# Kernel tuning notes

Measured on AMD Instinct MI355X. Metric: run time of the kernel, lower is better.

Reference implementation:

```python
import jax, jax.numpy as jnp
import numpy as np

VOCAB, HIDDEN, BATCH, TLEN = 32000, 512, 32, 64


def _lstm_cell(x, h, c, Wih, Whh, bih, bhh):
    # PyTorch LSTMCell gate order: i, f, g, o
    g = x @ Wih.T + bih + h @ Whh.T + bhh  # [B, 4H]
    i, f, gg, o = jnp.split(g, 4, axis=-1)
    i = jax.nn.sigmoid(i)
    f = jax.nn.sigmoid(f)
    gg = jnp.tanh(gg)
    o = jax.nn.sigmoid(o)
    c2 = f * c + i * gg
    h2 = o * jnp.tanh(c2)
    return h2, c2


def setup_inputs() -> dict:
    key = jax.random.key(0)
    ks = jax.random.split(key, 16)
    s = 0.02
    inp = {
        "inputs": jax.random.randint(ks[0], (1, BATCH), 0, VOCAB),
        "hiddens": jax.random.normal(ks[1], (BATCH, HIDDEN), jnp.float32),
        "target_sequences": jax.random.randint(ks[2], (BATCH, TLEN), 0, VOCAB),
        "use_tf": 1,
        "emb": jax.random.normal(ks[3], (VOCAB, HIDDEN), jnp.float32) * s,
        "W_ih1": jax.random.normal(ks[4], (4 * HIDDEN, HIDDEN), jnp.float32) * s,
        "W_hh1": jax.random.normal(ks[5], (4 * HIDDEN, HIDDEN), jnp.float32) * s,
        "b_ih1": jax.random.normal(ks[6], (4 * HIDDEN,), jnp.float32) * s,
        "b_hh1": jax.random.normal(ks[7], (4 * HIDDEN,), jnp.float32) * s,
        "W_ih2": jax.random.normal(ks[8], (4 * HIDDEN, HIDDEN), jnp.float32) * s,
        "W_hh2": jax.random.normal(ks[9], (4 * HIDDEN, HIDDEN), jnp.float32) * s,
        "b_ih2": jax.random.normal(ks[10], (4 * HIDDEN,), jnp.float32) * s,
        "b_hh2": jax.random.normal(ks[11], (4 * HIDDEN,), jnp.float32) * s,
        "W_out": jax.random.normal(ks[12], (VOCAB, HIDDEN), jnp.float32) * s,
        "b_out": jax.random.normal(ks[13], (VOCAB,), jnp.float32) * s,
    }
    return inp


def reference(inputs, hiddens, target_sequences, use_tf, emb, W_ih1, W_hh1,
              b_ih1, b_hh1, W_ih2, W_hh2, b_ih2, b_hh2, W_out, b_out):
    # Teacher-forcing path (use_tf is a static Python int; dropout p=0 -> identity).
    B = inputs.shape[1]
    H = hiddens.shape[1]
    # step i consumes: emb(inputs) for i=0, emb(target[:, i-1]) for i>0
    e0 = emb[inputs[0]]                              # [B, H]
    et = emb[target_sequences.T[:-1]]                # [T-1, B, H]
    x_seq = jnp.concatenate([e0[None], et], axis=0)  # [T, B, H]

    c1 = jnp.zeros((B, H), hiddens.dtype)
    h2 = jnp.zeros((B, H), hiddens.dtype)
    c2 = jnp.zeros((B, H), hiddens.dtype)

    def step(carry, x):
        h1, c1, h2, c2 = carry
        h1, c1 = _lstm_cell(x, h1, c1, W_ih1, W_hh1, b_ih1, b_hh1)
        h2, c2 = _lstm_cell(h1, h2, c2, W_ih2, W_hh2, b_ih2, b_hh2)
        probs = jax.nn.softmax(h2 @ W_out.T + b_out, axis=-1)  # [B, V]
        return (h1, c1, h2, c2), probs

    (h1, c1, h2, c2), output = jax.lax.scan(step, (hiddens, c1, h2, c2), x_seq)
    return output, h1  # output: [T, B, V]
```

## Files before the change

kernel.cpp:

```cpp
#include <hip/hip_runtime.h>
#include <stdint.h>


constexpr int kH = 512;
constexpr int kB = 32;
constexpr int kT = 64;
constexpr int kV = 32000;
constexpr int kG = 2048;
constexpr int kNWG = 256;
constexpr int kWS = 129;

typedef __attribute__((ext_vector_type(4))) float f4;
typedef __attribute__((ext_vector_type(8))) short short8;
typedef unsigned long long u64;

struct us4 { unsigned short x, y, z, w; };

__device__ inline unsigned short f2bf(float x) {
  union { float f; unsigned u; } c; c.f = x;
  unsigned r = c.u + 0x7fffu + ((c.u >> 16) & 1u);
  return (unsigned short)(r >> 16);
}
__device__ inline float sigm(float x) { return 1.0f / (1.0f + expf(-x)); }

__global__ void k_init(float* __restrict__ buf2, float* __restrict__ rowsum,
                       int* __restrict__ flags ) {
  int id = blockIdx.x * 256 + threadIdx.x;
  f4 z = {0.f, 0.f, 0.f, 0.f};
  if (id < 8192) ((f4*)buf2)[id] = z;
  if (id < 2048) rowsum[id] = 0.f;
  if (id < 512)  flags[id] = 0;
}

__global__ void k_wcvt(const float* __restrict__ W, unsigned short* __restrict__ Wu) {
  const int total = kV * kH / 4;
  for (int i = blockIdx.x * blockDim.x + threadIdx.x; i < total;
       i += gridDim.x * blockDim.x) {
    f4 v = ((const f4*)W)[i];
    us4 o = {f2bf(v.x), f2bf(v.y), f2bf(v.z), f2bf(v.w)};
    ((us4*)Wu)[i] = o;
  }
}

__global__ __launch_bounds__(256) void k_xg1(
    const int* __restrict__ inputs, const int* __restrict__ tseq,
    const float* __restrict__ emb, const float* __restrict__ Wih1,
    const float* __restrict__ bih1, const float* __restrict__ bhh1,
    float* __restrict__ Xg1T) {
  __shared__ float Xs[kB * kH];
  int tid = threadIdx.x;
  int t = blockIdx.x, jb = blockIdx.y;
  for (int i = tid; i < kB * kH / 4; i += 256) {
    int b = i >> 7;
    int tok = (t == 0) ? inputs[b] : tseq[b * kT + (t - 1)];
    ((f4*)Xs)[i] = ((const f4*)(emb + (size_t)tok * kH))[i & 127];
  }
  __syncthreads();
  int j2 = tid & 31, bq = tid >> 5;
  int j0 = jb * 64 + j2 * 2;
  int b0 = bq * 4;
  const f4* w0 = (const f4*)(Wih1 + (size_t)j0 * kH);
  const f4* w1 = (const f4*)(Wih1 + (size_t)(j0 + 1) * kH);
  float acc0[4] = {0.f, 0.f, 0.f, 0.f};
  float acc1[4] = {0.f, 0.f, 0.f, 0.f};
  #pragma unroll 2
  for (int k4 = 0; k4 < 128; ++k4) {
    f4 a0 = w0[k4], a1 = w1[k4];
    #pragma unroll
    for (int bb = 0; bb < 4; ++bb) {
      f4 x = ((const f4*)Xs)[(b0 + bb) * 128 + k4];
      acc0[bb] += a0.x * x.x + a0.y * x.y + a0.z * x.z + a0.w * x.w;
      acc1[bb] += a1.x * x.x + a1.y * x.y + a1.z * x.z + a1.w * x.w;
    }
  }
  float bj0 = bih1[j0] + bhh1[j0];
  float bj1 = bih1[j0 + 1] + bhh1[j0 + 1];
  f4 s0 = {acc0[0] + bj0, acc0[1] + bj0, acc0[2] + bj0, acc0[3] + bj0};
  f4 s1 = {acc1[0] + bj1, acc1[1] + bj1, acc1[2] + bj1, acc1[3] + bj1};
  float* o = Xg1T + ((size_t)t * kG + j0) * kB + b0;
  *(f4*)o = s0;
  *(f4*)(o + kB) = s1;
}

__device__ inline void postc(int* cnt) {
  __syncthreads();
  if (threadIdx.x == 0)
    __hip_atomic_fetch_add(&cnt[(blockIdx.x & 7) << 5], 1, __ATOMIC_RELAXED,
                           __HIP_MEMORY_SCOPE_AGENT);
}
__device__ inline void waitc(int* cnt, int target) {
  if (threadIdx.x < 64) {
    int lane = threadIdx.x;
    for (;;) {
      int v = (lane < 8)
                  ? __hip_atomic_load(&cnt[lane << 5], __ATOMIC_RELAXED,
                                      __HIP_MEMORY_SCOPE_AGENT)
                  : 0;
      v += __shfl_xor(v, 1);
      v += __shfl_xor(v, 2);
      v += __shfl_xor(v, 4);
      if (__shfl(v, 0) >= target) break;
      __builtin_amdgcn_s_sleep(2);
    }
  }
  __syncthreads();
}

__device__ inline void stage_coh(float* __restrict__ smem, const float* src) {
  const u64* s8 = (const u64*)src;
  #pragma unroll
  for (int i = 0; i < 16; ++i) {
    int idx = threadIdx.x + (i << 8);
    u64 lo = __hip_atomic_load((u64*)&s8[idx * 2], __ATOMIC_RELAXED,
                               __HIP_MEMORY_SCOPE_AGENT);
    u64 hi = __hip_atomic_load((u64*)&s8[idx * 2 + 1], __ATOMIC_RELAXED,
                               __HIP_MEMORY_SCOPE_AGENT);
    int b_ = idx >> 7, k4 = idx & 127;
    union { u64 u[2]; f4 v; } cv; cv.u[0] = lo; cv.u[1] = hi;
    ((f4*)smem)[(b_ << 7) + (k4 ^ (b_ & 7))] = cv.v;
  }
}
__device__ inline void stage_plain(float* __restrict__ smem,
                                   const float* __restrict__ src) {
  const f4* s4 = (const f4*)src;
  #pragma unroll
  for (int i = 0; i < 16; ++i) {
    int idx = threadIdx.x + (i << 8);
    int b_ = idx >> 7, k4 = idx & 127;
    ((f4*)smem)[(b_ << 7) + (k4 ^ (b_ & 7))] = s4[idx];
  }
}

__device__ inline float redk(float s) {
  s += __shfl_xor(s, 1);
  s += __shfl_xor(s, 2);
  s += __shfl_xor(s, 4);
  return s;
}

__global__ __launch_bounds__(256, 1) void k_serial(
    const float* __restrict__ hiddens, const float* __restrict__ Xg1T,
    const float* __restrict__ Whh1, const float* __restrict__ Wih2,
    const float* __restrict__ Whh2, const float* __restrict__ bih2,
    const float* __restrict__ bhh2,
    float* __restrict__ buf1, float* __restrict__ buf2,
    unsigned short* __restrict__ H2u, float* __restrict__ outTail,
    int* __restrict__ cntA, int* __restrict__ cntB) {
  __shared__ float smemh[kB * kH];
  __shared__ float wlds[24 * 4 * kWS];
  const int tid = threadIdx.x, w = blockIdx.x;
  const int lane = tid & 63, wv = tid >> 6;
  const int ks = lane & 7;
  const int nl = (lane >> 3) & 1;
  const int bq = lane >> 4;
  const int bp = (wv << 2) | bq;
  const int b0 = bp << 1, b1 = b0 + 1;
  const int b0off = b0 << 7, b1off = b1 << 7;
  const int b0sw = b0 & 7, b1sw = b1 & 7;
  const int n = (w << 1) + nl;

  {
    f4* wl = (f4*)wlds;
    #pragma unroll
    for (int i = 0; i < 12; ++i) {
      int idx = tid + (i << 8);
      int row = idx >> 7, k4 = idx & 127;
      int m = row >> 3, jjr = row & 7;
      int jr = ((jjr >> 1) << 9) + (w << 1) + (jjr & 1);
      const float* src = (m == 0) ? Whh1 : (m == 1) ? Whh2 : Wih2;
      wl[row * kWS + k4] = ((const f4*)(src + (size_t)jr * kH))[k4];
    }
  }
  const f4* wr_hh1[4];
  const f4* wr_hh2[4];
  const f4* wr_ih2[4];
  #pragma unroll
  for (int gg = 0; gg < 4; ++gg) {
    int row = 2 * gg + nl;
    wr_hh1[gg] = (const f4*)wlds + (0 * 8 + row) * kWS;
    wr_hh2[gg] = (const f4*)wlds + (1 * 8 + row) * kWS;
    wr_ih2[gg] = (const f4*)wlds + (2 * 8 + row) * kWS;
  }
  float bj[4];
  #pragma unroll
  for (int gg = 0; gg < 4; ++gg)
    bj[gg] = bih2[(gg << 9) + n] + bhh2[(gg << 9) + n];

  const f4* hsm = (const f4*)smemh;
  float c1a = 0.f, c1b = 0.f, c2a = 0.f, c2b = 0.f;
  const f4 z4 = {0.f, 0.f, 0.f, 0.f};

  stage_plain(smemh, hiddens);
  __syncthreads();
  for (int t = 0; t < kT; ++t) {
    float* h1w = buf1 + (t & 1) * 16384;
    float* h2w = buf2 + (t & 1) * 16384;
    const float* h2r = buf2 + ((t + 1) & 1) * 16384;

    union { u64 u; float f[2]; } xv[4];
    const float* xbase = Xg1T + ((size_t)t * kG + n) * kB + b0;
    #pragma unroll
    for (int gg = 0; gg < 4; ++gg)
      xv[gg].u = *(const u64*)(xbase + (size_t)(gg << 9) * kB);

    f4 a00 = z4, a01 = z4, a10 = z4, a11 = z4, a20 = z4, a21 = z4,
       a30 = z4, a31 = z4;
    #pragma unroll 4
    for (int kk = 0; kk < 16; ++kk) {
      int k4 = (kk << 3) | ks;
      f4 h0v = hsm[b0off + (k4 ^ b0sw)];
      f4 h1v = hsm[b1off + (k4 ^ b1sw)];
      f4 w0 = wr_hh1[0][k4], w1 = wr_hh1[1][k4];
      f4 w2 = wr_hh1[2][k4], w3 = wr_hh1[3][k4];
      a00 += w0 * h0v; a01 += w0 * h1v;
      a10 += w1 * h0v; a11 += w1 * h1v;
      a20 += w2 * h0v; a21 += w2 * h1v;
      a30 += w3 * h0v; a31 += w3 * h1v;
    }
    float G00 = redk(a00.x + a00.y + a00.z + a00.w) + xv[0].f[0];
    float G01 = redk(a01.x + a01.y + a01.z + a01.w) + xv[0].f[1];
    float G10 = redk(a10.x + a10.y + a10.z + a10.w) + xv[1].f[0];
    float G11 = redk(a11.x + a11.y + a11.z + a11.w) + xv[1].f[1];
    float G20 = redk(a20.x + a20.y + a20.z + a20.w) + xv[2].f[0];
    float G21 = redk(a21.x + a21.y + a21.z + a21.w) + xv[2].f[1];
    float G30 = redk(a30.x + a30.y + a30.z + a30.w) + xv[3].f[0];
    float G31 = redk(a31.x + a31.y + a31.z + a31.w) + xv[3].f[1];
    c1a = sigm(G10) * c1a + sigm(G00) * tanhf(G20);
    float hn0 = sigm(G30) * tanhf(c1a);
    c1b = sigm(G11) * c1b + sigm(G01) * tanhf(G21);
    float hn1 = sigm(G31) * tanhf(c1b);
    float hp0 = __shfl(hn0, lane ^ 8);
    float hp1 = __shfl(hn1, lane ^ 8);
    if ((lane & 15) == 0) {
      union { float f[2]; u64 u; } p0, p1;
      p0.f[0] = hn0; p0.f[1] = hp0;
      p1.f[0] = hn1; p1.f[1] = hp1;
      __hip_atomic_store((u64*)(h1w + b0 * kH + 2 * w), p0.u, __ATOMIC_RELAXED,
                         __HIP_MEMORY_SCOPE_AGENT);
      __hip_atomic_store((u64*)(h1w + b1 * kH + 2 * w), p1.u, __ATOMIC_RELAXED,
                         __HIP_MEMORY_SCOPE_AGENT);
      if (t == kT - 1) {
        *(u64*)(outTail + b0 * kH + 2 * w) = p0.u;
        *(u64*)(outTail + b1 * kH + 2 * w) = p1.u;
      }
    }
    postc(cntA);
    waitc(cntB, 256 * t);

    stage_coh(smemh, h2r);
    __syncthreads();
    a00 = z4; a01 = z4; a10 = z4; a11 = z4;
    a20 = z4; a21 = z4; a30 = z4; a31 = z4;
    #pragma unroll 4
    for (int kk = 0; kk < 16; ++kk) {
      int k4 = (kk << 3) | ks;
      f4 h0v = hsm[b0off + (k4 ^ b0sw)];
      f4 h1v = hsm[b1off + (k4 ^ b1sw)];
      f4 w0 = wr_hh2[0][k4], w1 = wr_hh2[1][k4];
      f4 w2 = wr_hh2[2][k4], w3 = wr_hh2[3][k4];
      a00 += w0 * h0v; a01 += w0 * h1v;
      a10 += w1 * h0v; a11 += w1 * h1v;
      a20 += w2 * h0v; a21 += w2 * h1v;
      a30 += w3 * h0v; a31 += w3 * h1v;
    }
    waitc(cntA, 256 * (t + 1));

    stage_coh(smemh, h1w);
    __syncthreads();
    #pragma unroll 4
    for (int kk = 0; kk < 16; ++kk) {
      int k4 = (kk << 3) | ks;
      f4 h0v = hsm[b0off + (k4 ^ b0sw)];
      f4 h1v = hsm[b1off + (k4 ^ b1sw)];
      f4 w0 = wr_ih2[0][k4], w1 = wr_ih2[1][k4];
      f4 w2 = wr_ih2[2][k4], w3 = wr_ih2[3][k4];
      a00 += w0 * h0v; a01 += w0 * h1v;
      a10 += w1 * h0v; a11 += w1 * h1v;
      a20 += w2 * h0v; a21 += w2 * h1v;
      a30 += w3 * h0v; a31 += w3 * h1v;
    }
    G00 = redk(a00.x + a00.y + a00.z + a00.w) + bj[0];
    G01 = redk(a01.x + a01.y + a01.z + a01.w) + bj[0];
    G10 = redk(a10.x + a10.y + a10.z + a10.w) + bj[1];
    G11 = redk(a11.x + a11.y + a11.z + a11.w) + bj[1];
    G20 = redk(a20.x + a20.y + a20.z + a20.w) + bj[2];
    G21 = redk(a21.x + a21.y + a21.z + a21.w) + bj[2];
    G30 = redk(a30.x + a30.y + a30.z + a30.w) + bj[3];
    G31 = redk(a31.x + a31.y + a31.z + a31.w) + bj[3];
    c2a = sigm(G10) * c2a + sigm(G00) * tanhf(G20);
    float h2n0 = sigm(G30) * tanhf(c2a);
    c2b = sigm(G11) * c2b + sigm(G01) * tanhf(G21);
    float h2n1 = sigm(G31) * tanhf(c2b);
    float h2p0 = __shfl(h2n0, lane ^ 8);
    float h2p1 = __shfl(h2n1, lane ^ 8);
    if ((lane & 15) == 0) {
      union { float f[2]; u64 u; } p0, p1;
      p0.f[0] = h2n0; p0.f[1] = h2p0;
      p1.f[0] = h2n1; p1.f[1] = h2p1;
      __hip_atomic_store((u64*)(h2w + b0 * kH + 2 * w), p0.u, __ATOMIC_RELAXED,
                         __HIP_MEMORY_SCOPE_AGENT);
      __hip_atomic_store((u64*)(h2w + b1 * kH + 2 * w), p1.u, __ATOMIC_RELAXED,
                         __HIP_MEMORY_SCOPE_AGENT);
      unsigned bf0 = ((unsigned)f2bf(h2p0) << 16) | f2bf(h2n0);
      unsigned bf1 = ((unsigned)f2bf(h2p1) << 16) | f2bf(h2n1);
      *(unsigned*)(H2u + ((size_t)t * kB + b0) * kH + 2 * w) = bf0;
      *(unsigned*)(H2u + ((size_t)t * kB + b1) * kH + 2 * w) = bf1;
    }
    postc(cntB);
  }
}

__global__ __launch_bounds__(256) void k_vocab(
    const unsigned short* __restrict__ H2u, const unsigned short* __restrict__ Wu,
    const float* __restrict__ bout, float* __restrict__ out,
    float* __restrict__ rowsum) {
  const int lane = threadIdx.x & 63, wv = threadIdx.x >> 6;
  const int wm = wv >> 1, wn = wv & 1;
  const int r16 = lane & 15, quad = lane >> 4;
  const int mBase = blockIdx.y * 128 + wm * 64;
  const int nBase = blockIdx.x * 128 + wn * 64;
  f4 acc[4][4];
  #pragma unroll
  for (int a = 0; a < 4; ++a)
    #pragma unroll
    for (int c = 0; c < 4; ++c) acc[a][c] = (f4){0.f, 0.f, 0.f, 0.f};
  for (int kb = 0; kb < 16; ++kb) {
    int k0 = kb * 32 + quad * 8;
    short8 af[4], bf[4];
    #pragma unroll
    for (int mt = 0; mt < 4; ++mt)
      af[mt] = *(const short8*)(H2u + (size_t)(mBase + mt * 16 + r16) * kH + k0);
    #pragma unroll
    for (int nt = 0; nt < 4; ++nt)
      bf[nt] = *(const short8*)(Wu + (size_t)(nBase + nt * 16 + r16) * kH + k0);
    #pragma unroll
    for (int mt = 0; mt < 4; ++mt)
      #pragma unroll
      for (int nt = 0; nt < 4; ++nt)
        acc[mt][nt] = __builtin_amdgcn_mfma_f32_16x16x32_bf16(
            af[mt], bf[nt], acc[mt][nt], 0, 0, 0);
  }
  float bo[4];
  #pragma unroll
  for (int nt = 0; nt < 4; ++nt) bo[nt] = bout[nBase + nt * 16 + r16];
  #pragma unroll
  for (int mt = 0; mt < 4; ++mt) {
    #pragma unroll
    for (int r = 0; r < 4; ++r) {
      int row = mBase + mt * 16 + quad * 4 + r;
      float s = 0.f;
      #pragma unroll
      for (int nt = 0; nt < 4; ++nt) {
        float p = __expf(acc[mt][nt][r] + bo[nt]);
        out[(size_t)row * kV + nBase + nt * 16 + r16] = p;
        s += p;
      }
      s += __shfl_xor(s, 1);
      s += __shfl_xor(s, 2);
      s += __shfl_xor(s, 4);
      s += __shfl_xor(s, 8);
      if (r16 == 0) atomicAdd(&rowsum[row], s);
    }
  }
}

__global__ void k_scale(float* __restrict__ out, const float* __restrict__ rowsum) {
  const unsigned total4 = (unsigned)(kT * kB) * (kV / 4);
  unsigned stride = gridDim.x * blockDim.x;
  for (unsigned i = blockIdx.x * blockDim.x + threadIdx.x; i < total4; i += stride) {
    unsigned row = i / (kV / 4);
    float inv = 1.0f / rowsum[row];
    f4 v = ((const f4*)out)[i];
    ((f4*)out)[i] = v * inv;
  }
}

extern "C" void kernel_launch(void* const* d_in, const int* in_sizes, int n_in,
                              void* d_out, int out_size, void* d_ws, size_t ws_size,
                              hipStream_t stream) {
  (void)in_sizes; (void)n_in; (void)out_size; (void)ws_size;
  const int*   inputs  = (const int*)d_in[0];
  const float* hiddens = (const float*)d_in[1];
  const int*   tseq    = (const int*)d_in[2];
  const float* emb  = (const float*)d_in[4];
  const float* Wih1 = (const float*)d_in[5];
  const float* Whh1 = (const float*)d_in[6];
  const float* bih1 = (const float*)d_in[7];
  const float* bhh1 = (const float*)d_in[8];
  const float* Wih2 = (const float*)d_in[9];
  const float* Whh2 = (const float*)d_in[10];
  const float* bih2 = (const float*)d_in[11];
  const float* bhh2 = (const float*)d_in[12];
  const float* Wout = (const float*)d_in[13];
  const float* bout = (const float*)d_in[14];

  float* ws = (float*)d_ws;
  float* Xg1T = ws;
  float* buf1 = ws + 4194304;
  float* buf2 = ws + 4227072;
  unsigned short* H2u = (unsigned short*)(ws + 4259840);
  unsigned short* Wu  = (unsigned short*)(ws + 4784128);
  float* rowsum = ws + 12976128;
  int* flags = (int*)(ws + 12978176);
  int* cntA = flags;
  int* cntB = flags + 256;

  float* out = (float*)d_out;
  float* outTail = out + (size_t)kT * kB * kV;

  hipLaunchKernelGGL(k_init, dim3(32), dim3(256), 0, stream, buf2, rowsum, flags);
  hipLaunchKernelGGL(k_wcvt, dim3(1024), dim3(256), 0, stream, Wout, Wu);
  hipLaunchKernelGGL(k_xg1, dim3(64, 32), dim3(256), 0, stream,
                     inputs, tseq, emb, Wih1, bih1, bhh1, Xg1T);
  hipLaunchKernelGGL(k_serial, dim3(kNWG), dim3(256), 0, stream,
                     hiddens, Xg1T, Whh1, Wih2, Whh2, bih2, bhh2,
                     buf1, buf2, H2u, outTail, cntA, cntB);
  hipLaunchKernelGGL(k_vocab, dim3(kV / 128, 16), dim3(256), 0, stream,
                     H2u, Wu, bout, out, rowsum);
  hipLaunchKernelGGL(k_scale, dim3(2048), dim3(256), 0, stream, out, rowsum);
}
```

Before: 2.072 ms.

## Fuse vocab projection and softmax normalization into the persistent recurrent kernel

Removes the separate vocab GEMM and scale kernels. Each of 250 persistent workgroups now computes a 32x128 logits tile for step t-1 while waiting on the recurrence, and writes normalized probabilities for step t-2 after the existing inter-WG barrier. Partial row sums go to per-WG slots and are summed on read. This hides vocab work behind the latency-bound serial loop and avoids writing then re-reading the unnormalized output. In exchange it adds MFMA work and register pressure inside the critical serial loop, which may lengthen each step.

```diff
diff --git a/kernel.cpp b/kernel.cpp
--- a/kernel.cpp
+++ b/kernel.cpp
@@ -9,6 +9,7 @@
 constexpr int kG = 2048;
 constexpr int kNWG = 256;
 constexpr int kWS = 129;
+constexpr int kNV = 250;
 
 typedef __attribute__((ext_vector_type(4))) float f4;
 typedef __attribute__((ext_vector_type(8))) short short8;
@@ -23,12 +24,12 @@
 }
 __device__ inline float sigm(float x) { return 1.0f / (1.0f + expf(-x)); }
 
-__global__ void k_init(float* __restrict__ buf2, float* __restrict__ rowsum,
+__global__ void k_init(float* __restrict__ buf2, float* __restrict__ rs,
                        int* __restrict__ flags ) {
   int id = blockIdx.x * 256 + threadIdx.x;
   f4 z = {0.f, 0.f, 0.f, 0.f};
   if (id < 8192) ((f4*)buf2)[id] = z;
-  if (id < 2048) rowsum[id] = 0.f;
+  ((f4*)rs)[id] = z;
   if (id < 512)  flags[id] = 0;
 }
 
@@ -144,10 +145,14 @@
     const float* __restrict__ Whh2, const float* __restrict__ bih2,
     const float* __restrict__ bhh2,
     float* __restrict__ buf1, float* __restrict__ buf2,
-    unsigned short* __restrict__ H2u, float* __restrict__ outTail,
+    unsigned short* __restrict__ H2u,
+    const unsigned short* __restrict__ Wu, const float* __restrict__ bout,
+    float* __restrict__ outP, float* __restrict__ rs,
+    float* __restrict__ outTail,
     int* __restrict__ cntA, int* __restrict__ cntB) {
   __shared__ float smemh[kB * kH];
   __shared__ float wlds[24 * 4 * kWS];
+  __shared__ float sinv[4][32];
   const int tid = threadIdx.x, w = blockIdx.x;
   const int lane = tid & 63, wv = tid >> 6;
   const int ks = lane & 7;
@@ -158,6 +163,10 @@
   const int b0off = b0 << 7, b1off = b1 << 7;
   const int b0sw = b0 & 7, b1sw = b1 & 7;
   const int n = (w << 1) + nl;
+  const int r16 = lane & 15, quad = lane >> 4;
+  const int colb = w * 128 + wv * 32;
+  float bo0 = 0.f, bo1 = 0.f;
+  if (w < kNV) { bo0 = bout[colb + r16]; bo1 = bout[colb + 16 + r16]; }
 
   {
     f4* wl = (f4*)wlds;
@@ -189,6 +198,83 @@
   const f4* hsm = (const f4*)smemh;
   float c1a = 0.f, c1b = 0.f, c2a = 0.f, c2b = 0.f;
   const f4 z4 = {0.f, 0.f, 0.f, 0.f};
+  f4 p00 = z4, p01 = z4, p10 = z4, p11 = z4;
+
+  auto vocab_tile = [&](int tt) {
+    p00 = z4; p01 = z4; p10 = z4; p11 = z4;
+    const unsigned short* A0 = H2u + ((size_t)tt * kB + r16) * kH;
+    const unsigned short* A1 = A0 + (size_t)16 * kH;
+    const unsigned short* B0 = Wu + (size_t)(colb + r16) * kH;
+    const unsigned short* B1 = B0 + (size_t)16 * kH;
+    #pragma unroll 2
+    for (int kb = 0; kb < 16; ++kb) {
+      int k0 = kb * 32 + quad * 8;
+      union { u64 u[2]; short8 s; } a0, a1;
+      a0.u[0] = __hip_atomic_load((const u64*)(A0 + k0), __ATOMIC_RELAXED,
+                                  __HIP_MEMORY_SCOPE_AGENT);
+      a0.u[1] = __hip_atomic_load((const u64*)(A0 + k0 + 4), __ATOMIC_RELAXED,
+                                  __HIP_MEMORY_SCOPE_AGENT);
+      a1.u[0] = __hip_atomic_load((const u64*)(A1 + k0), __ATOMIC_RELAXED,
+                                  __HIP_MEMORY_SCOPE_AGENT);
+      a1.u[1] = __hip_atomic_load((const u64*)(A1 + k0 + 4), __ATOMIC_RELAXED,
+                                  __HIP_MEMORY_SCOPE_AGENT);
+      short8 vb0 = *(const short8*)(B0 + k0);
+      short8 vb1 = *(const short8*)(B1 + k0);
+      p00 = __builtin_amdgcn_mfma_f32_16x16x32_bf16(a0.s, vb0, p00, 0, 0, 0);
+      p01 = __builtin_amdgcn_mfma_f32_16x16x32_bf16(a0.s, vb1, p01, 0, 0, 0);
+      p10 = __builtin_amdgcn_mfma_f32_16x16x32_bf16(a1.s, vb0, p10, 0, 0, 0);
+      p11 = __builtin_amdgcn_mfma_f32_16x16x32_bf16(a1.s, vb1, p11, 0, 0, 0);
+    }
+    float* rsb = rs + tt * 1024 + (w & 31) * 32;
+    #pragma unroll
+    for (int r = 0; r < 4; ++r) {
+      float e0 = __expf(p00[r] + bo0), e1 = __expf(p01[r] + bo1);
+      p00[r] = e0; p01[r] = e1;
+      float s = e0 + e1;
+      s += __shfl_xor(s, 1); s += __shfl_xor(s, 2);
+      s += __shfl_xor(s, 4); s += __shfl_xor(s, 8);
+      if (r16 == 0) atomicAdd(&rsb[quad * 4 + r], s);
+      float f0 = __expf(p10[r] + bo0), f1 = __expf(p11[r] + bo1);
+      p10[r] = f0; p11[r] = f1;
+      float u = f0 + f1;
+      u += __shfl_xor(u, 1); u += __shfl_xor(u, 2);
+      u += __shfl_xor(u, 4); u += __shfl_xor(u, 8);
+      if (r16 == 0) atomicAdd(&rsb[16 + quad * 4 + r], u);
+    }
+  };
+  auto scale_store = [&](int ts) {
+    const float* rb = rs + ts * 1024;
+    if (lane < 32) {
+      float s = 0.f;
+      #pragma unroll 8
+      for (int sl = 0; sl < 32; ++sl) {
+        union { unsigned u; float f; } cv;
+        cv.u = __hip_atomic_load((const unsigned*)(rb + sl * 32 + lane),
+                                 __ATOMIC_RELAXED, __HIP_MEMORY_SCOPE_AGENT);
+        s += cv.f;
+      }
+      sinv[wv][lane] = 1.0f / s;
+    }
+    __syncthreads();
+    float* ob = outP + (size_t)ts * kB * kV + colb;
+    #pragma unroll
+    for (int r = 0; r < 4; ++r) {
+      {
+        int rr = quad * 4 + r;
+        float inv = sinv[wv][rr];
+        float* orow = ob + (size_t)rr * kV;
+        orow[r16] = p00[r] * inv;
+        orow[16 + r16] = p01[r] * inv;
+      }
+      {
+        int rr = 16 + quad * 4 + r;
+        float inv = sinv[wv][rr];
+        float* orow = ob + (size_t)rr * kV;
+        orow[r16] = p10[r] * inv;
+        orow[16 + r16] = p11[r] * inv;
+      }
+    }
+  };
 
   stage_plain(smemh, hiddens);
   __syncthreads();
@@ -232,23 +318,28 @@
     float hp0 = __shfl(hn0, lane ^ 8);
     float hp1 = __shfl(hn1, lane ^ 8);
     if ((lane & 15) == 0) {
-      union { float f[2]; u64 u; } p0, p1;
-      p0.f[0] = hn0; p0.f[1] = hp0;
-      p1.f[0] = hn1; p1.f[1] = hp1;
-      __hip_atomic_store((u64*)(h1w + b0 * kH + 2 * w), p0.u, __ATOMIC_RELAXED,
+      union { float f[2]; u64 u; } q0, q1;
+      q0.f[0] = hn0; q0.f[1] = hp0;
+      q1.f[0] = hn1; q1.f[1] = hp1;
+      __hip_atomic_store((u64*)(h1w + b0 * kH + 2 * w), q0.u, __ATOMIC_RELAXED,
                          __HIP_MEMORY_SCOPE_AGENT);
-      __hip_atomic_store((u64*)(h1w + b1 * kH + 2 * w), p1.u, __ATOMIC_RELAXED,
+      __hip_atomic_store((u64*)(h1w + b1 * kH + 2 * w), q1.u, __ATOMIC_RELAXED,
                          __HIP_MEMORY_SCOPE_AGENT);
       if (t == kT - 1) {
-        *(u64*)(outTail + b0 * kH + 2 * w) = p0.u;
-        *(u64*)(outTail + b1 * kH + 2 * w) = p1.u;
+        *(u64*)(outTail + b0 * kH + 2 * w) = q0.u;
+        *(u64*)(outTail + b1 * kH + 2 * w) = q1.u;
       }
     }
     postc(cntA);
     waitc(cntB, 256 * t);
 
+    if (t >= 2 && w < kNV) scale_store(t - 2);
+
     stage_coh(smemh, h2r);
     __syncthreads();
+
+    if (t >= 1 && w < kNV) vocab_tile(t - 1);
+
     a00 = z4; a01 = z4; a10 = z4; a11 = z4;
     a20 = z4; a21 = z4; a30 = z4; a31 = z4;
     #pragma unroll 4
@@ -294,85 +385,29 @@
     float h2p0 = __shfl(h2n0, lane ^ 8);
     float h2p1 = __shfl(h2n1, lane ^ 8);
     if ((lane & 15) == 0) {
-      union { float f[2]; u64 u; } p0, p1;
-      p0.f[0] = h2n0; p0.f[1] = h2p0;
-      p1.f[0] = h2n1; p1.f[1] = h2p1;
-      __hip_atomic_store((u64*)(h2w + b0 * kH + 2 * w), p0.u, __ATOMIC_RELAXED,
+      union { float f[2]; u64 u; } q0, q1;
+      q0.f[0] = h2n0; q0.f[1] = h2p0;
+      q1.f[0] = h2n1; q1.f[1] = h2p1;
+      __hip_atomic_store((u64*)(h2w + b0 * kH + 2 * w), q0.u, __ATOMIC_RELAXED,
                          __HIP_MEMORY_SCOPE_AGENT);
-      __hip_atomic_store((u64*)(h2w + b1 * kH + 2 * w), p1.u, __ATOMIC_RELAXED,
+      __hip_atomic_store((u64*)(h2w + b1 * kH + 2 * w), q1.u, __ATOMIC_RELAXED,
                          __HIP_MEMORY_SCOPE_AGENT);
       unsigned bf0 = ((unsigned)f2bf(h2p0) << 16) | f2bf(h2n0);
       unsigned bf1 = ((unsigned)f2bf(h2p1) << 16) | f2bf(h2n1);
-      *(unsigned*)(H2u + ((size_t)t * kB + b0) * kH + 2 * w) = bf0;
-      *(unsigned*)(H2u + ((size_t)t * kB + b1) * kH + 2 * w) = bf1;
+      __hip_atomic_store((unsigned*)(H2u + ((size_t)t * kB + b0) * kH + 2 * w),
+                         bf0, __ATOMIC_RELAXED, __HIP_MEMORY_SCOPE_AGENT);
+      __hip_atomic_store((unsigned*)(H2u + ((size_t)t * kB + b1) * kH + 2 * w),
+                         bf1, __ATOMIC_RELAXED, __HIP_MEMORY_SCOPE_AGENT);
     }
     postc(cntB);
   }
-}
-
-__global__ __launch_bounds__(256) void k_vocab(
-    const unsigned short* __restrict__ H2u, const unsigned short* __restrict__ Wu,
-    const float* __restrict__ bout, float* __restrict__ out,
-    float* __restrict__ rowsum) {
-  const int lane = threadIdx.x & 63, wv = threadIdx.x >> 6;
-  const int wm = wv >> 1, wn = wv & 1;
-  const int r16 = lane & 15, quad = lane >> 4;
-  const int mBase = blockIdx.y * 128 + wm * 64;
-  const int nBase = blockIdx.x * 128 + wn * 64;
-  f4 acc[4][4];
-  #pragma unroll
-  for (int a = 0; a < 4; ++a)
-    #pragma unroll
-    for (int c = 0; c < 4; ++c) acc[a][c] = (f4){0.f, 0.f, 0.f, 0.f};
-  for (int kb = 0; kb < 16; ++kb) {
-    int k0 = kb * 32 + quad * 8;
-    short8 af[4], bf[4];
-    #pragma unroll
-    for (int mt = 0; mt < 4; ++mt)
-      af[mt] = *(const short8*)(H2u + (size_t)(mBase + mt * 16 + r16) * kH + k0);
-    #pragma unroll
-    for (int nt = 0; nt < 4; ++nt)
-      bf[nt] = *(const short8*)(Wu + (size_t)(nBase + nt * 16 + r16) * kH + k0);
-    #pragma unroll
-    for (int mt = 0; mt < 4; ++mt)
-      #pragma unroll
-      for (int nt = 0; nt < 4; ++nt)
-        acc[mt][nt] = __builtin_amdgcn_mfma_f32_16x16x32_bf16(
-            af[mt], bf[nt], acc[mt][nt], 0, 0, 0);
-  }
-  float bo[4];
-  #pragma unroll
-  for (int nt = 0; nt < 4; ++nt) bo[nt] = bout[nBase + nt * 16 + r16];
-  #pragma unroll
-  for (int mt = 0; mt < 4; ++mt) {
-    #pragma unroll
-    for (int r = 0; r < 4; ++r) {
-      int row = mBase + mt * 16 + quad * 4 + r;
-      float s = 0.f;
-      #pragma unroll
-      for (int nt = 0; nt < 4; ++nt) {
-        float p = __expf(acc[mt][nt][r] + bo[nt]);
-        out[(size_t)row * kV + nBase + nt * 16 + r16] = p;
-        s += p;
-      }
-      s += __shfl_xor(s, 1);
-      s += __shfl_xor(s, 2);
-      s += __shfl_xor(s, 4);
-      s += __shfl_xor(s, 8);
-      if (r16 == 0) atomicAdd(&rowsum[row], s);
-    }
-  }
-}
-
-__global__ void k_scale(float* __restrict__ out, const float* __restrict__ rowsum) {
-  const unsigned total4 = (unsigned)(kT * kB) * (kV / 4);
-  unsigned stride = gridDim.x * blockDim.x;
-  for (unsigned i = blockIdx.x * blockDim.x + threadIdx.x; i < total4; i += stride) {
-    unsigned row = i / (kV / 4);
-    float inv = 1.0f / rowsum[row];
-    f4 v = ((const f4*)out)[i];
-    ((f4*)out)[i] = v * inv;
-  }
+
+  waitc(cntB, 256 * kT);
+  if (w < kNV) scale_store(kT - 2);
+  if (w < kNV) vocab_tile(kT - 1);
+  postc(cntA);
+  waitc(cntA, 256 * (kT + 1));
+  if (w < kNV) scale_store(kT - 1);
 }
 
 extern "C" void kernel_launch(void* const* d_in, const int* in_sizes, int n_in,
@@ -400,22 +435,19 @@
   float* buf2 = ws + 4227072;
   unsigned short* H2u = (unsigned short*)(ws + 4259840);
   unsigned short* Wu  = (unsigned short*)(ws + 4784128);
-  float* rowsum = ws + 12976128;
-  int* flags = (int*)(ws + 12978176);
+  float* rs = ws + 12976128;
+  int* flags = (int*)(ws + 13041664);
   int* cntA = flags;
   int* cntB = flags + 256;
 
   float* out = (float*)d_out;
   float* outTail = out + (size_t)kT * kB * kV;
 
-  hipLaunchKernelGGL(k_init, dim3(32), dim3(256), 0, stream, buf2, rowsum, flags);
+  hipLaunchKernelGGL(k_init, dim3(64), dim3(256), 0, stream, buf2, rs, flags);
   hipLaunchKernelGGL(k_wcvt, dim3(1024), dim3(256), 0, stream, Wout, Wu);
   hipLaunchKernelGGL(k_xg1, dim3(64, 32), dim3(256), 0, stream,
                      inputs, tseq, emb, Wih1, bih1, bhh1, Xg1T);
   hipLaunchKernelGGL(k_serial, dim3(kNWG), dim3(256), 0, stream,
                      hiddens, Xg1T, Whh1, Wih2, Whh2, bih2, bhh2,
-                     buf1, buf2, H2u, outTail, cntA, cntB);
-  hipLaunchKernelGGL(k_vocab, dim3(kV / 128, 16), dim3(256), 0, stream,
-                     H2u, Wu, bout, out, rowsum);
-  hipLaunchKernelGGL(k_scale, dim3(2048), dim3(256), 0, stream, out, rowsum);
-}
+                     buf1, buf2, H2u, Wu, bout, out, rs, outTail, cntA, cntB);
+}
```

After: 2.468 ms. +19.1%, slower.
